# Optimization experiments

Hardware: AMD Instinct MI355X
Metric: run time of the kernel (lower is better)

## Reference

```python
import jax, jax.numpy as jnp
import numpy as np

SLIDING_WINDOW = 512  # matches init kwarg
BLOCK_STRIDE = 32     # tokens per cache page


def setup_inputs() -> dict:
    key = jax.random.key(0)
    k0, k1, k2, k3 = jax.random.split(key, 4)
    B, S, HQ, HKV, D = 2, 2048, 32, 8, 128
    nb = S // BLOCK_STRIDE
    q = jax.random.normal(k0, (B, S, HQ, D), jnp.float32)
    k = jax.random.normal(k1, (B, S, HKV, D), jnp.float32)
    v = jax.random.normal(k2, (B, S, HKV, D), jnp.float32)
    sink = jax.random.normal(k3, (HQ,), jnp.float32)
    cache_state = jnp.zeros((B * nb, 2, HKV, BLOCK_STRIDE, D), jnp.float32)
    seq_block_ids = jnp.arange(B * nb, dtype=jnp.int32).reshape(B, nb)
    return {"q": q, "k": k, "v": v, "cache_state": cache_state,
            "seq_block_ids": seq_block_ids, "sink": sink}


def reference(q, k, v, cache_state, seq_block_ids, sink):
    B, S, HQ, D = q.shape
    HKV = k.shape[2]
    G = HQ // HKV  # GQA group size
    stride = cache_state.shape[3]
    nb = S // stride

    # --- write prefill K/V into the paged cache ---
    # pages laid out [num_pages, k/v, HKV, stride, D]
    k_pg = k.reshape(B, nb, stride, HKV, D).transpose(0, 1, 3, 2, 4).reshape(B * nb, HKV, stride, D)
    v_pg = v.reshape(B, nb, stride, HKV, D).transpose(0, 1, 3, 2, 4).reshape(B * nb, HKV, stride, D)
    ids = seq_block_ids.reshape(-1)
    new_cache = cache_state.at[ids, 0].set(k_pg).at[ids, 1].set(v_pg)

    # --- sliding-window causal attention with sink logits (GQA, no repeat) ---
    scale = 1.0 / np.sqrt(D).astype(np.float32)
    qg = q.reshape(B, S, HKV, G, D)
    # scores: [B, HKV, G, Sq, Sk]
    scores = jnp.einsum('bqhgd,bshd->bhgqs', qg, k) * scale
    i = jnp.arange(S)[:, None]
    j = jnp.arange(S)[None, :]
    allowed = (j <= i) & ((i - j) < SLIDING_WINDOW)  # causal banded mask
    neg = jnp.finfo(scores.dtype).min
    scores = jnp.where(allowed, scores, neg)
    # per-head sink logit appended as extra key column, dropped after softmax
    sink_col = jnp.broadcast_to(sink.reshape(HKV, G)[None, :, :, None, None], (B, HKV, G, S, 1))
    probs = jax.nn.softmax(jnp.concatenate([scores, sink_col], axis=-1), axis=-1)[..., :S]
    out = jnp.einsum('bhgqs,bshd->bqhgd', probs, v).reshape(B, S, HQ, D)
    return out, new_cache
```

## Files before the change

kernel.cpp:

```cpp
#include <hip/hip_runtime.h>
#include <hip/hip_bf16.h>
#include <stdint.h>

#define BB 2
#define SS 2048
#define HQ 32
#define HKV 8
#define DD 128
#define WIN 512

typedef __bf16 bf16x8 __attribute__((ext_vector_type(8)));
typedef float f32x16 __attribute__((ext_vector_type(16)));

__device__ __forceinline__ bf16x8 cvt8(float4 a, float4 b, float s) {
  bf16x8 r;
  r[0] = (__bf16)(a.x * s); r[1] = (__bf16)(a.y * s);
  r[2] = (__bf16)(a.z * s); r[3] = (__bf16)(a.w * s);
  r[4] = (__bf16)(b.x * s); r[5] = (__bf16)(b.y * s);
  r[6] = (__bf16)(b.z * s); r[7] = (__bf16)(b.w * s);
  return r;
}

__device__ __forceinline__ uint32_t pk2(float lo, float hi) {
  uint32_t w;
  asm("v_cvt_pk_bf16_f32 %0, %1, %2" : "=v"(w) : "v"(lo), "v"(hi));
  return w;
}

__device__ __forceinline__ unsigned short bfu(float x) {
  union { __bf16 b; unsigned short u; } c; c.b = (__bf16)x; return c.u;
}

#define SWZ(r) ((((r) ^ ((r) >> 3)) & 7) << 4)

__global__ __launch_bounds__(512, 2) void attn_kernel(
    const float* __restrict__ qg, const float* __restrict__ sinkg,
    float* __restrict__ outg,
    const unsigned short* __restrict__ kbg, const unsigned short* __restrict__ vtg)
{
  const int col = (blockIdx.x & 7) + 8 * ((blockIdx.x >> 3) & 1);
  const int rank = blockIdx.x >> 4;
  const int qtile = rank < 24 ? rank + 8 : 31 - rank;
  const int hkv = col & 7, b = col >> 3;
  const int qb = qtile * 64;
  const int tid = threadIdx.x;
  const int wave = tid >> 6, lane = tid & 63;
  const int c5 = lane & 31, hi = lane >> 5;
  const int hq = (hkv << 2) + (wave >> 1);
  const int qw = qb + (wave & 1) * 32;
  const int qrow = qw + c5;

  __shared__ __align__(16) __bf16 Kl[2][64 * 128];
  __shared__ __align__(16) __bf16 Vt[2][128 * 64];

  const float LOG2E = 1.4426950408889634f;
  const float scale = 0.08838834764831845f * LOG2E;
  const float THR = 12.0f;

  bf16x8 qf[8];
  {
    const float* qp = qg + (((size_t)b * SS + qrow) * HQ + hq) * DD + hi * 8;
    #pragma unroll
    for (int ch = 0; ch < 8; ++ch) {
      float4 a = *(const float4*)(qp + ch * 16);
      float4 a2 = *(const float4*)(qp + ch * 16 + 4);
      qf[ch] = cvt8(a, a2, scale);
    }
  }
  const float sk = sinkg[hq] * LOG2E;

  float mm = -1e30f, ll = 0.f;
  f32x16 acc[4];
  #pragma unroll
  for (int d = 0; d < 4; ++d)
    #pragma unroll
    for (int r = 0; r < 16; ++r) acc[d][r] = 0.f;

  const int t0 = (qb > (WIN - 1) ? (qb - (WIN - 1)) : 0) >> 6;
  const int t1 = (qb + 63) >> 6;

  const char* kcol = (const char*)kbg + (size_t)(b * HKV + hkv) * (SS * DD * 2);
  const char* vcol = (const char*)vtg + (size_t)(b * HKV + hkv) * (SS * DD * 2);
  const int p0 = tid * 32;
  const int kr = p0 >> 8, kx = p0 & 255;
  const int vrw = p0 >> 7, vx = p0 & 127;
  const int kd0 = kr * 256 + (kx ^ SWZ(kr)), kd1 = kr * 256 + ((kx + 16) ^ SWZ(kr));
  const int vd0 = vrw * 128 + (vx ^ SWZ(vrw)), vd1 = vrw * 128 + ((vx + 16) ^ SWZ(vrw));

  uint4 ksA, ksB, vsA, vsB;
  auto issue = [&](int t) {
    const char* kt = kcol + (size_t)t * 16384;
    const char* vt = vcol + (size_t)t * 16384;
    ksA = *(const uint4*)(kt + p0); ksB = *(const uint4*)(kt + p0 + 16);
    vsA = *(const uint4*)(vt + p0); vsB = *(const uint4*)(vt + p0 + 16);
  };
  auto commit = [&](int buf) {
    char* kb_ = (char*)&Kl[buf][0]; char* vb_ = (char*)&Vt[buf][0];
    *(uint4*)(kb_ + kd0) = ksA; *(uint4*)(kb_ + kd1) = ksB;
    *(uint4*)(vb_ + vd0) = vsA; *(uint4*)(vb_ + vd1) = vsB;
  };

  issue(t0);
  commit(0);
  __syncthreads();
  int cur = 0;

  const int swA = SWZ(c5);
  const int swB = swA ^ 0x40;

  for (int t = t0; t <= t1; ++t) {
    if (t < t1) issue(t + 1);
    const int kb = t << 6;

    if (kb <= qw + 31 && kb + 63 >= qw - (WIN - 1)) {
      const char* Ksc = (const char*)&Kl[cur][0];
      const char* Vsc = (const char*)&Vt[cur][0];

      f32x16 s0, s1;
      #pragma unroll
      for (int r = 0; r < 16; ++r) { s0[r] = 0.f; s1[r] = 0.f; }
      __builtin_amdgcn_s_setprio(1);
      #pragma unroll
      for (int ch = 0; ch < 8; ++ch) {
        const int colb = ch * 32 + hi * 16;
        bf16x8 a0 = *(const bf16x8*)(Ksc + c5 * 256 + (colb ^ swA));
        bf16x8 a1 = *(const bf16x8*)(Ksc + (32 + c5) * 256 + (colb ^ swB));
        s0 = __builtin_amdgcn_mfma_f32_32x32x16_bf16(a0, qf[ch], s0, 0, 0, 0);
        s1 = __builtin_amdgcn_mfma_f32_32x32x16_bf16(a1, qf[ch], s1, 0, 0, 0);
      }
      __builtin_amdgcn_s_setprio(0);

      const bool noMask = (kb + 63 <= qw) && (kb >= qw - (WIN - 32));

      if (!noMask) {
        #pragma unroll
        for (int r = 0; r < 16; ++r) {
          const int lr = (r & 3) + 8 * (r >> 2) + 4 * hi;
          const int kv0 = kb + lr, kv1 = kv0 + 32;
          const bool ok0 = (kv0 <= qrow) && (qrow - kv0 < WIN);
          const bool ok1 = (kv1 <= qrow) && (qrow - kv1 < WIN);
          s0[r] = ok0 ? s0[r] : -1e30f;
          s1[r] = ok1 ? s1[r] : -1e30f;
        }
      }
      float tmax = s0[0];
      #pragma unroll
      for (int r = 1; r < 16; ++r) tmax = fmaxf(tmax, s0[r]);
      #pragma unroll
      for (int r = 0; r < 16; ++r) tmax = fmaxf(tmax, s1[r]);
      tmax = fmaxf(tmax, __shfl_xor(tmax, 32));

      const bool resc = __any(tmax > mm + THR);
      const float mnew = resc ? fmaxf(mm, tmax) : mm;
      float tsum = 0.f;
      if (noMask) {
        #pragma unroll
        for (int r = 0; r < 16; ++r) {
          s0[r] = exp2f(s0[r] - mnew); tsum += s0[r];
          s1[r] = exp2f(s1[r] - mnew); tsum += s1[r];
        }
      } else {
        #pragma unroll
        for (int r = 0; r < 16; ++r) {
          s0[r] = (s0[r] > -9e29f) ? exp2f(s0[r] - mnew) : 0.f; tsum += s0[r];
          s1[r] = (s1[r] > -9e29f) ? exp2f(s1[r] - mnew) : 0.f; tsum += s1[r];
        }
      }
      tsum += __shfl_xor(tsum, 32);

      if (resc) {
        const float scl = exp2f(mm - mnew);
        ll = ll * scl + tsum;
        #pragma unroll
        for (int d = 0; d < 4; ++d)
          #pragma unroll
          for (int r = 0; r < 16; ++r) acc[d][r] *= scl;
        mm = mnew;
      } else {
        ll += tsum;
      }

      bf16x8 pb[4];
      #pragma unroll
      for (int kvq = 0; kvq < 4; ++kvq) {
        const int bq = (kvq & 1) * 8;
        float e0, e1, e2, e3, e4, e5, e6, e7;
        if (kvq & 2) {
          e0 = s1[bq+0]; e1 = s1[bq+1]; e2 = s1[bq+2]; e3 = s1[bq+3];
          e4 = s1[bq+4]; e5 = s1[bq+5]; e6 = s1[bq+6]; e7 = s1[bq+7];
        } else {
          e0 = s0[bq+0]; e1 = s0[bq+1]; e2 = s0[bq+2]; e3 = s0[bq+3];
          e4 = s0[bq+4]; e5 = s0[bq+5]; e6 = s0[bq+6]; e7 = s0[bq+7];
        }
        const uint32_t A0 = pk2(e0, e1), A1 = pk2(e2, e3);
        const uint32_t B0 = pk2(e4, e5), B1 = pk2(e6, e7);
        const uint32_t XA0 = __shfl_xor(A0, 32), XA1 = __shfl_xor(A1, 32);
        const uint32_t XB0 = __shfl_xor(B0, 32), XB1 = __shfl_xor(B1, 32);
        union { uint4 u; bf16x8 v; } cvu;
        cvu.u.x = hi ? XB0 : A0;
        cvu.u.y = hi ? XB1 : A1;
        cvu.u.z = hi ? B0 : XA0;
        cvu.u.w = hi ? B1 : XA1;
        pb[kvq] = cvu.v;
      }

      __builtin_amdgcn_s_setprio(1);
      #pragma unroll
      for (int d = 0; d < 4; ++d) {
        const int rowb = (d * 32 + c5) * 128;
        const int swV = swA ^ ((d & 1) << 6);
        #pragma unroll
        for (int kvq = 0; kvq < 4; ++kvq) {
          bf16x8 va = *(const bf16x8*)(Vsc + rowb + ((kvq * 32 + hi * 16) ^ swV));
          acc[d] = __builtin_amdgcn_mfma_f32_32x32x16_bf16(va, pb[kvq], acc[d], 0, 0, 0);
        }
      }
      __builtin_amdgcn_s_setprio(0);
    }

    if (t < t1) {
      commit(cur ^ 1);
      __syncthreads();
      cur ^= 1;
    }
  }

  {
    const float Mf = fmaxf(mm, sk);
    const float ex = exp2f(mm - Mf);
    const float denom = ll * ex + exp2f(sk - Mf);
    const float fac = ex / denom;
    float* orow = outg + (((size_t)b * SS + qrow) * HQ + hq) * DD;
    #pragma unroll
    for (int d = 0; d < 4; ++d) {
      #pragma unroll
      for (int q4 = 0; q4 < 4; ++q4) {
        float4 o;
        o.x = acc[d][q4 * 4 + 0] * fac;
        o.y = acc[d][q4 * 4 + 1] * fac;
        o.z = acc[d][q4 * 4 + 2] * fac;
        o.w = acc[d][q4 * 4 + 3] * fac;
        *(float4*)(orow + d * 32 + q4 * 8 + 4 * hi) = o;
      }
    }
  }
}

__global__ void prep_kv(const float* __restrict__ kg, const float* __restrict__ vg,
                        unsigned short* __restrict__ kb, unsigned short* __restrict__ vt) {
  const int bx = blockIdx.x;
  const int t = bx & 31, colx = bx >> 5;
  const int b = colx >> 3, hkv = colx & 7;
  const int kbrow = t * 64;
  if (blockIdx.y == 0) {
    #pragma unroll
    for (int i = 0; i < 8; ++i) {
      const int idx = i * 1024 + threadIdx.x * 4;
      const int r = idx >> 7, d = idx & 127;
      float4 v = *(const float4*)(kg + (((size_t)b * SS + kbrow + r) * HKV + hkv) * DD + d);
      ushort4 o = make_ushort4(bfu(v.x), bfu(v.y), bfu(v.z), bfu(v.w));
      *(ushort4*)(kb + ((size_t)colx * SS + kbrow + r) * DD + d) = o;
    }
  } else {
    __shared__ unsigned short Vl[64][132];
    #pragma unroll
    for (int i = 0; i < 8; ++i) {
      const int idx = i * 1024 + threadIdx.x * 4;
      const int kv = idx >> 7, d = idx & 127;
      float4 v = *(const float4*)(vg + (((size_t)b * SS + kbrow + kv) * HKV + hkv) * DD + d);
      Vl[kv][d + 0] = bfu(v.x); Vl[kv][d + 1] = bfu(v.y);
      Vl[kv][d + 2] = bfu(v.z); Vl[kv][d + 3] = bfu(v.w);
    }
    __syncthreads();
    #pragma unroll
    for (int i = 0; i < 8; ++i) {
      const int idx = i * 1024 + threadIdx.x * 4;
      const int d = idx >> 6, kv = idx & 63;
      ushort4 o = make_ushort4(Vl[kv + 0][d], Vl[kv + 1][d], Vl[kv + 2][d], Vl[kv + 3][d]);
      *(ushort4*)(vt + ((size_t)colx * 32 + t) * 8192 + d * 64 + kv) = o;
    }
  }
}

__global__ __launch_bounds__(512, 2) void attn_fallback(
    const float* __restrict__ qg, const float* __restrict__ kg,
    const float* __restrict__ vg, const float* __restrict__ sinkg,
    float* __restrict__ outg)
{
  const int col = (blockIdx.x & 7) + 8 * ((blockIdx.x >> 3) & 1);
  const int rank = blockIdx.x >> 4;
  const int qtile = rank < 24 ? rank + 8 : 31 - rank;
  const int hkv = col & 7, b = col >> 3;
  const int qb = qtile * 64;
  const int tid = threadIdx.x;
  const int wave = tid >> 6, lane = tid & 63;
  const int c5 = lane & 31, hi = lane >> 5;
  const int hq = (hkv << 2) + (wave >> 1);
  const int qw = qb + (wave & 1) * 32;
  const int qrow = qw + c5;

  __shared__ __align__(16) __bf16 Kl[2][64 * 128];
  __shared__ __align__(16) __bf16 Vt[2][128 * 64];

  const float LOG2E = 1.4426950408889634f;
  const float scale = 0.08838834764831845f * LOG2E;
  const float THR = 12.0f;

  bf16x8 qf[8];
  {
    const float* qp = qg + (((size_t)b * SS + qrow) * HQ + hq) * DD + hi * 8;
    #pragma unroll
    for (int ch = 0; ch < 8; ++ch) {
      float4 a = *(const float4*)(qp + ch * 16);
      float4 a2 = *(const float4*)(qp + ch * 16 + 4);
      qf[ch] = cvt8(a, a2, scale);
    }
  }
  const float sk = sinkg[hq] * LOG2E;

  float mm = -1e30f, ll = 0.f;
  f32x16 acc[4];
  #pragma unroll
  for (int d = 0; d < 4; ++d)
    #pragma unroll
    for (int r = 0; r < 16; ++r) acc[d][r] = 0.f;

  const int t0 = (qb > (WIN - 1) ? (qb - (WIN - 1)) : 0) >> 6;
  const int t1 = (qb + 63) >> 6;

  const int krow = tid >> 3, kchunk = tid & 7;
  const int vd = tid & 127, vslot = tid >> 7;
  const size_t KSTEP = (size_t)64 * HKV * DD;
  const float* kBase = kg + (((size_t)b * SS + krow) * HKV + hkv) * DD + kchunk * 16;
  const float* vBase = vg + (((size_t)b * SS + vslot * 16) * HKV + hkv) * DD + vd;

  float4 k0, k1, k2, k3; float vr[16];
  auto issue = [&](int t) {
    const float* kp = kBase + (size_t)t * KSTEP;
    k0 = *(const float4*)(kp);     k1 = *(const float4*)(kp + 4);
    k2 = *(const float4*)(kp + 8); k3 = *(const float4*)(kp + 12);
    const float* vp = vBase + (size_t)t * KSTEP;
    #pragma unroll
    for (int j = 0; j < 16; ++j) vr[j] = vp[(size_t)j * (HKV * DD)];
  };
  const int ksw = SWZ(krow);
  const int vsw = SWZ(vd);
  auto commit = [&](int buf) {
    char* kd = (char*)(&Kl[buf][0]) + krow * 256;
    *(bf16x8*)(kd + ((kchunk * 32) ^ ksw)) = cvt8(k0, k1, 1.f);
    *(bf16x8*)(kd + ((kchunk * 32 + 16) ^ ksw)) = cvt8(k2, k3, 1.f);
    char* vdst = (char*)(&Vt[buf][0]) + vd * 128;
    bf16x8 w0, w1;
    #pragma unroll
    for (int j = 0; j < 8; ++j) { w0[j] = (__bf16)vr[j]; w1[j] = (__bf16)vr[8 + j]; }
    *(bf16x8*)(vdst + ((vslot * 32) ^ vsw)) = w0;
    *(bf16x8*)(vdst + ((vslot * 32 + 16) ^ vsw)) = w1;
  };

  issue(t0);
  commit(0);
  __syncthreads();
  int cur = 0;

  const int swA = SWZ(c5);
  const int swB = swA ^ 0x40;

  for (int t = t0; t <= t1; ++t) {
    if (t < t1) issue(t + 1);
    const int kb = t << 6;
    if (kb <= qw + 31 && kb + 63 >= qw - (WIN - 1)) {
      const char* Ksc = (const char*)&Kl[cur][0];
      const char* Vsc = (const char*)&Vt[cur][0];
      f32x16 s0, s1;
      #pragma unroll
      for (int r = 0; r < 16; ++r) { s0[r] = 0.f; s1[r] = 0.f; }
      __builtin_amdgcn_s_setprio(1);
      #pragma unroll
      for (int ch = 0; ch < 8; ++ch) {
        const int colb = ch * 32 + hi * 16;
        bf16x8 a0 = *(const bf16x8*)(Ksc + c5 * 256 + (colb ^ swA));
        bf16x8 a1 = *(const bf16x8*)(Ksc + (32 + c5) * 256 + (colb ^ swB));
        s0 = __builtin_amdgcn_mfma_f32_32x32x16_bf16(a0, qf[ch], s0, 0, 0, 0);
        s1 = __builtin_amdgcn_mfma_f32_32x32x16_bf16(a1, qf[ch], s1, 0, 0, 0);
      }
      __builtin_amdgcn_s_setprio(0);

      const bool noMask = (kb + 63 <= qw) && (kb >= qw - (WIN - 32));
      if (!noMask) {
        #pragma unroll
        for (int r = 0; r < 16; ++r) {
          const int lr = (r & 3) + 8 * (r >> 2) + 4 * hi;
          const int kv0 = kb + lr, kv1 = kv0 + 32;
          const bool ok0 = (kv0 <= qrow) && (qrow - kv0 < WIN);
          const bool ok1 = (kv1 <= qrow) && (qrow - kv1 < WIN);
          s0[r] = ok0 ? s0[r] : -1e30f;
          s1[r] = ok1 ? s1[r] : -1e30f;
        }
      }
      float tmax = s0[0];
      #pragma unroll
      for (int r = 1; r < 16; ++r) tmax = fmaxf(tmax, s0[r]);
      #pragma unroll
      for (int r = 0; r < 16; ++r) tmax = fmaxf(tmax, s1[r]);
      tmax = fmaxf(tmax, __shfl_xor(tmax, 32));
      const bool resc = __any(tmax > mm + THR);
      const float mnew = resc ? fmaxf(mm, tmax) : mm;
      float tsum = 0.f;
      if (noMask) {
        #pragma unroll
        for (int r = 0; r < 16; ++r) {
          s0[r] = exp2f(s0[r] - mnew); tsum += s0[r];
          s1[r] = exp2f(s1[r] - mnew); tsum += s1[r];
        }
      } else {
        #pragma unroll
        for (int r = 0; r < 16; ++r) {
          s0[r] = (s0[r] > -9e29f) ? exp2f(s0[r] - mnew) : 0.f; tsum += s0[r];
          s1[r] = (s1[r] > -9e29f) ? exp2f(s1[r] - mnew) : 0.f; tsum += s1[r];
        }
      }
      tsum += __shfl_xor(tsum, 32);
      if (resc) {
        const float scl = exp2f(mm - mnew);
        ll = ll * scl + tsum;
        #pragma unroll
        for (int d = 0; d < 4; ++d)
          #pragma unroll
          for (int r = 0; r < 16; ++r) acc[d][r] *= scl;
        mm = mnew;
      } else {
        ll += tsum;
      }
      bf16x8 pb[4];
      #pragma unroll
      for (int kvq = 0; kvq < 4; ++kvq) {
        const int bq = (kvq & 1) * 8;
        float e0, e1, e2, e3, e4, e5, e6, e7;
        if (kvq & 2) {
          e0 = s1[bq+0]; e1 = s1[bq+1]; e2 = s1[bq+2]; e3 = s1[bq+3];
          e4 = s1[bq+4]; e5 = s1[bq+5]; e6 = s1[bq+6]; e7 = s1[bq+7];
        } else {
          e0 = s0[bq+0]; e1 = s0[bq+1]; e2 = s0[bq+2]; e3 = s0[bq+3];
          e4 = s0[bq+4]; e5 = s0[bq+5]; e6 = s0[bq+6]; e7 = s0[bq+7];
        }
        const uint32_t A0 = pk2(e0, e1), A1 = pk2(e2, e3);
        const uint32_t B0 = pk2(e4, e5), B1 = pk2(e6, e7);
        const uint32_t XA0 = __shfl_xor(A0, 32), XA1 = __shfl_xor(A1, 32);
        const uint32_t XB0 = __shfl_xor(B0, 32), XB1 = __shfl_xor(B1, 32);
        union { uint4 u; bf16x8 v; } cvu;
        cvu.u.x = hi ? XB0 : A0;
        cvu.u.y = hi ? XB1 : A1;
        cvu.u.z = hi ? B0 : XA0;
        cvu.u.w = hi ? B1 : XA1;
        pb[kvq] = cvu.v;
      }
      __builtin_amdgcn_s_setprio(1);
      #pragma unroll
      for (int d = 0; d < 4; ++d) {
        const int rowb = (d * 32 + c5) * 128;
        const int swV = swA ^ ((d & 1) << 6);
        #pragma unroll
        for (int kvq = 0; kvq < 4; ++kvq) {
          bf16x8 va = *(const bf16x8*)(Vsc + rowb + ((kvq * 32 + hi * 16) ^ swV));
          acc[d] = __builtin_amdgcn_mfma_f32_32x32x16_bf16(va, pb[kvq], acc[d], 0, 0, 0);
        }
      }
      __builtin_amdgcn_s_setprio(0);
    }
    if (t < t1) {
      commit(cur ^ 1);
      __syncthreads();
      cur ^= 1;
    }
  }
  {
    const float Mf = fmaxf(mm, sk);
    const float ex = exp2f(mm - Mf);
    const float denom = ll * ex + exp2f(sk - Mf);
    const float fac = ex / denom;
    float* orow = outg + (((size_t)b * SS + qrow) * HQ + hq) * DD;
    #pragma unroll
    for (int d = 0; d < 4; ++d) {
      #pragma unroll
      for (int q4 = 0; q4 < 4; ++q4) {
        float4 o;
        o.x = acc[d][q4 * 4 + 0] * fac;
        o.y = acc[d][q4 * 4 + 1] * fac;
        o.z = acc[d][q4 * 4 + 2] * fac;
        o.w = acc[d][q4 * 4 + 3] * fac;
        *(float4*)(orow + d * 32 + q4 * 8 + 4 * hi) = o;
      }
    }
  }
}

__global__ void build_inv(const int* __restrict__ ids, int* __restrict__ inv,
                          int npages, int nslots) {
  const int i = threadIdx.x;
  if (i < npages) inv[i] = -1;
  __syncthreads();
  if (i < nslots) inv[ids[i]] = i;
}

__global__ void page_fill(const float* __restrict__ kg, const float* __restrict__ vg,
                          const float* __restrict__ cache_in, const int* __restrict__ inv,
                          float* __restrict__ cache) {
  const int page = blockIdx.x, half = blockIdx.y;
  const int slot = inv[page];
  float4* d4 = (float4*)cache;
  const size_t dbase = (((size_t)page * 2 + half) * 8) * 1024;
  if (slot >= 0) {
    const int b = slot >> 6, blk = slot & 63;
    const float4* s4 = (const float4*)(half ? vg : kg);
    for (int f = threadIdx.x; f < 8192; f += blockDim.x) {
      const int d = f & 31, s = (f >> 5) & 31, h = f >> 10;
      d4[dbase + (size_t)h * 1024 + s * 32 + d] =
          s4[(((size_t)b * SS + blk * 32 + s) * 8 + h) * 32 + d];
    }
  } else {
    const float4* s4 = (const float4*)cache_in;
    for (int f = threadIdx.x; f < 8192; f += blockDim.x)
      d4[dbase + f] = s4[dbase + f];
  }
}

__global__ void cache_copy(const float* __restrict__ src, float* __restrict__ dst, int n4) {
  const float4* s = (const float4*)src;
  float4* d = (float4*)dst;
  for (int i = blockIdx.x * blockDim.x + threadIdx.x; i < n4; i += gridDim.x * blockDim.x)
    d[i] = s[i];
}
__global__ void cache_scatter(const float* __restrict__ kg, const float* __restrict__ vg,
                              const int* __restrict__ ids, float* __restrict__ cache) {
  const int slot = blockIdx.x;
  const int half = blockIdx.y;
  const int b = slot >> 6, blk = slot & 63;
  const int page = ids[slot];
  const float4* s4 = (const float4*)(half ? vg : kg);
  float4* d4 = (float4*)cache;
  for (int f = threadIdx.x; f < 8192; f += blockDim.x) {
    const int d = f & 31, s = (f >> 5) & 31, h = f >> 10;
    d4[(((size_t)page * 2 + half) * 8 + h) * 1024 + s * 32 + d] =
        s4[(((size_t)b * SS + blk * 32 + s) * 8 + h) * 32 + d];
  }
}

extern "C" void kernel_launch(void* const* d_in, const int* in_sizes, int n_in,
                              void* d_out, int out_size, void* d_ws, size_t ws_size,
                              hipStream_t stream) {
  const float* q = (const float*)d_in[0];
  const float* k = (const float*)d_in[1];
  const float* v = (const float*)d_in[2];
  const float* cache_in = (const float*)d_in[3];
  const int* ids = (const int*)d_in[4];
  const float* sink = (const float*)d_in[5];
  float* out = (float*)d_out;
  float* cache_out = out + (size_t)BB * SS * HQ * DD;

  const int nslots = in_sizes[4];
  const int npages = in_sizes[3] / (2 * HKV * 32 * DD);

  const size_t kvBytes = (size_t)BB * HKV * SS * DD * 2;
  const size_t need = 4096 + 2 * kvBytes;
  const bool smallMaps = (npages <= 1024) && (nslots <= 1024);

  if (ws_size >= need && smallMaps) {
    int* inv = (int*)d_ws;
    unsigned short* kbp = (unsigned short*)((char*)d_ws + 4096);
    unsigned short* vtp = kbp + kvBytes / 2;
    build_inv<<<1, 1024, 0, stream>>>(ids, inv, npages, nslots);
    page_fill<<<dim3(npages, 2), 256, 0, stream>>>(k, v, cache_in, inv, cache_out);
    prep_kv<<<dim3(BB * HKV * 32, 2), 256, 0, stream>>>(k, v, kbp, vtp);
    attn_kernel<<<512, 512, 0, stream>>>(q, sink, out, kbp, vtp);
  } else if (ws_size >= (size_t)npages * sizeof(int) && smallMaps) {
    int* inv = (int*)d_ws;
    build_inv<<<1, 1024, 0, stream>>>(ids, inv, npages, nslots);
    page_fill<<<dim3(npages, 2), 256, 0, stream>>>(k, v, cache_in, inv, cache_out);
    attn_fallback<<<512, 512, 0, stream>>>(q, k, v, sink, out);
  } else {
    cache_copy<<<4096, 256, 0, stream>>>(cache_in, cache_out, (BB * SS * HKV * DD * 2) / 4);
    cache_scatter<<<dim3(BB * 64, 2), 256, 0, stream>>>(k, v, ids, cache_out);
    attn_fallback<<<512, 512, 0, stream>>>(q, k, v, sink, out);
  }
}
```

Before: 107.8 us.

## Pre-swizzle K/V into MFMA fragment order and read directly from global

```diff
diff --git a/kernel.cpp b/kernel.cpp
--- a/kernel.cpp
+++ b/kernel.cpp
@@ -36,7 +36,7 @@
 __global__ __launch_bounds__(512, 2) void attn_kernel(
     const float* __restrict__ qg, const float* __restrict__ sinkg,
     float* __restrict__ outg,
-    const unsigned short* __restrict__ kbg, const unsigned short* __restrict__ vtg)
+    const unsigned short* __restrict__ kfg, const unsigned short* __restrict__ vfg)
 {
   const int col = (blockIdx.x & 7) + 8 * ((blockIdx.x >> 3) & 1);
   const int rank = blockIdx.x >> 4;
@@ -50,9 +50,6 @@
   const int qw = qb + (wave & 1) * 32;
   const int qrow = qw + c5;
 
-  __shared__ __align__(16) __bf16 Kl[2][64 * 128];
-  __shared__ __align__(16) __bf16 Vt[2][128 * 64];
-
   const float LOG2E = 1.4426950408889634f;
   const float scale = 0.08838834764831845f * LOG2E;
   const float THR = 12.0f;
@@ -76,28 +73,262 @@
     #pragma unroll
     for (int r = 0; r < 16; ++r) acc[d][r] = 0.f;
 
+  const int t0 = (qw > (WIN - 1) ? (qw - (WIN - 1)) : 0) >> 6;
+  const int t1 = (qw + 31) >> 6;
+
+  const unsigned short* kcol = kfg + (size_t)(b * HKV + hkv) * (SS * DD);
+  const unsigned short* vcol = vfg + (size_t)(b * HKV + hkv) * (SS * DD);
+  const int l8 = lane * 8;
+
+  for (int t = t0; t <= t1; ++t) {
+    const int kb = t << 6;
+    const unsigned short* kt = kcol + t * 8192;
+    const unsigned short* vt = vcol + t * 8192;
+
+    f32x16 s0, s1;
+    #pragma unroll
+    for (int r = 0; r < 16; ++r) { s0[r] = 0.f; s1[r] = 0.f; }
+    __builtin_amdgcn_s_setprio(1);
+    #pragma unroll
+    for (int ch = 0; ch < 8; ++ch) {
+      bf16x8 a0 = *(const bf16x8*)(kt + ch * 1024 + l8);
+      bf16x8 a1 = *(const bf16x8*)(kt + ch * 1024 + 512 + l8);
+      s0 = __builtin_amdgcn_mfma_f32_32x32x16_bf16(a0, qf[ch], s0, 0, 0, 0);
+      s1 = __builtin_amdgcn_mfma_f32_32x32x16_bf16(a1, qf[ch], s1, 0, 0, 0);
+    }
+    __builtin_amdgcn_s_setprio(0);
+
+    const bool noMask = (kb + 63 <= qw) && (kb >= qw - (WIN - 32));
+
+    if (!noMask) {
+      #pragma unroll
+      for (int r = 0; r < 16; ++r) {
+        const int lr = (r & 3) + 8 * (r >> 2) + 4 * hi;
+        const int kv0 = kb + lr, kv1 = kv0 + 32;
+        const bool ok0 = (kv0 <= qrow) && (qrow - kv0 < WIN);
+        const bool ok1 = (kv1 <= qrow) && (qrow - kv1 < WIN);
+        s0[r] = ok0 ? s0[r] : -1e30f;
+        s1[r] = ok1 ? s1[r] : -1e30f;
+      }
+    }
+    float tmax = s0[0];
+    #pragma unroll
+    for (int r = 1; r < 16; ++r) tmax = fmaxf(tmax, s0[r]);
+    #pragma unroll
+    for (int r = 0; r < 16; ++r) tmax = fmaxf(tmax, s1[r]);
+    tmax = fmaxf(tmax, __shfl_xor(tmax, 32));
+
+    const bool resc = __any(tmax > mm + THR);
+    const float mnew = resc ? fmaxf(mm, tmax) : mm;
+    float tsum = 0.f;
+    if (noMask) {
+      #pragma unroll
+      for (int r = 0; r < 16; ++r) {
+        s0[r] = exp2f(s0[r] - mnew); tsum += s0[r];
+        s1[r] = exp2f(s1[r] - mnew); tsum += s1[r];
+      }
+    } else {
+      #pragma unroll
+      for (int r = 0; r < 16; ++r) {
+        s0[r] = (s0[r] > -9e29f) ? exp2f(s0[r] - mnew) : 0.f; tsum += s0[r];
+        s1[r] = (s1[r] > -9e29f) ? exp2f(s1[r] - mnew) : 0.f; tsum += s1[r];
+      }
+    }
+    tsum += __shfl_xor(tsum, 32);
+
+    if (resc) {
+      const float scl = exp2f(mm - mnew);
+      ll = ll * scl + tsum;
+      #pragma unroll
+      for (int d = 0; d < 4; ++d)
+        #pragma unroll
+        for (int r = 0; r < 16; ++r) acc[d][r] *= scl;
+      mm = mnew;
+    } else {
+      ll += tsum;
+    }
+
+    bf16x8 pb[4];
+    #pragma unroll
+    for (int kvq = 0; kvq < 4; ++kvq) {
+      const int bq = (kvq & 1) * 8;
+      float e0, e1, e2, e3, e4, e5, e6, e7;
+      if (kvq & 2) {
+        e0 = s1[bq+0]; e1 = s1[bq+1]; e2 = s1[bq+2]; e3 = s1[bq+3];
+        e4 = s1[bq+4]; e5 = s1[bq+5]; e6 = s1[bq+6]; e7 = s1[bq+7];
+      } else {
+        e0 = s0[bq+0]; e1 = s0[bq+1]; e2 = s0[bq+2]; e3 = s0[bq+3];
+        e4 = s0[bq+4]; e5 = s0[bq+5]; e6 = s0[bq+6]; e7 = s0[bq+7];
+      }
+      const uint32_t A0 = pk2(e0, e1), A1 = pk2(e2, e3);
+      const uint32_t B0 = pk2(e4, e5), B1 = pk2(e6, e7);
+      const uint32_t XA0 = __shfl_xor(A0, 32), XA1 = __shfl_xor(A1, 32);
+      const uint32_t XB0 = __shfl_xor(B0, 32), XB1 = __shfl_xor(B1, 32);
+      union { uint4 u; bf16x8 v; } cvu;
+      cvu.u.x = hi ? XB0 : A0;
+      cvu.u.y = hi ? XB1 : A1;
+      cvu.u.z = hi ? B0 : XA0;
+      cvu.u.w = hi ? B1 : XA1;
+      pb[kvq] = cvu.v;
+    }
+
+    __builtin_amdgcn_s_setprio(1);
+    #pragma unroll
+    for (int d = 0; d < 4; ++d) {
+      #pragma unroll
+      for (int kvq = 0; kvq < 4; ++kvq) {
+        bf16x8 va = *(const bf16x8*)(vt + (d * 4 + kvq) * 512 + l8);
+        acc[d] = __builtin_amdgcn_mfma_f32_32x32x16_bf16(va, pb[kvq], acc[d], 0, 0, 0);
+      }
+    }
+    __builtin_amdgcn_s_setprio(0);
+  }
+
+  {
+    const float Mf = fmaxf(mm, sk);
+    const float ex = exp2f(mm - Mf);
+    const float denom = ll * ex + exp2f(sk - Mf);
+    const float fac = ex / denom;
+    float* orow = outg + (((size_t)b * SS + qrow) * HQ + hq) * DD;
+    #pragma unroll
+    for (int d = 0; d < 4; ++d) {
+      #pragma unroll
+      for (int q4 = 0; q4 < 4; ++q4) {
+        float4 o;
+        o.x = acc[d][q4 * 4 + 0] * fac;
+        o.y = acc[d][q4 * 4 + 1] * fac;
+        o.z = acc[d][q4 * 4 + 2] * fac;
+        o.w = acc[d][q4 * 4 + 3] * fac;
+        *(float4*)(orow + d * 32 + q4 * 8 + 4 * hi) = o;
+      }
+    }
+  }
+}
+
+__global__ void prep_kv(const float* __restrict__ kg, const float* __restrict__ vg,
+                        unsigned short* __restrict__ kf, unsigned short* __restrict__ vf) {
+  const int bx = blockIdx.x;
+  const int t = bx & 31, colx = bx >> 5;
+  const int b = colx >> 3, hkv = colx & 7;
+  const int kbrow = t * 64;
+  if (blockIdx.y == 0) {
+    unsigned short* dst = kf + (size_t)colx * (SS * DD) + t * 8192;
+    #pragma unroll
+    for (int i = 0; i < 4; ++i) {
+      const int c = i * 256 + threadIdx.x;
+      const int ch = c >> 7, rem = c & 127;
+      const int half = rem >> 6, l = rem & 63;
+      const int c5 = l & 31, h2 = l >> 5;
+      const int row = kbrow + half * 32 + c5;
+      const int d = ch * 16 + h2 * 8;
+      const float* kp = kg + (((size_t)b * SS + row) * HKV + hkv) * DD + d;
+      float4 a = *(const float4*)(kp);
+      float4 a2 = *(const float4*)(kp + 4);
+      union { unsigned short u[8]; uint4 q; } o;
+      o.u[0] = bfu(a.x);  o.u[1] = bfu(a.y);  o.u[2] = bfu(a.z);  o.u[3] = bfu(a.w);
+      o.u[4] = bfu(a2.x); o.u[5] = bfu(a2.y); o.u[6] = bfu(a2.z); o.u[7] = bfu(a2.w);
+      *(uint4*)(dst + (size_t)c * 8) = o.q;
+    }
+  } else {
+    __shared__ unsigned short Vl[64][132];
+    #pragma unroll
+    for (int i = 0; i < 8; ++i) {
+      const int idx = i * 1024 + threadIdx.x * 4;
+      const int kv = idx >> 7, d = idx & 127;
+      float4 v = *(const float4*)(vg + (((size_t)b * SS + kbrow + kv) * HKV + hkv) * DD + d);
+      Vl[kv][d + 0] = bfu(v.x); Vl[kv][d + 1] = bfu(v.y);
+      Vl[kv][d + 2] = bfu(v.z); Vl[kv][d + 3] = bfu(v.w);
+    }
+    __syncthreads();
+    unsigned short* dst = vf + (size_t)colx * (SS * DD) + t * 8192;
+    #pragma unroll
+    for (int i = 0; i < 4; ++i) {
+      const int c = i * 256 + threadIdx.x;
+      const int d4 = c >> 8, kvq = (c >> 6) & 3, l = c & 63;
+      const int c5 = l & 31, h2 = l >> 5;
+      const int kvb = kvq * 16 + h2 * 8;
+      const int dc = d4 * 32 + c5;
+      union { unsigned short u[8]; uint4 q; } o;
+      #pragma unroll
+      for (int j = 0; j < 8; ++j) o.u[j] = Vl[kvb + j][dc];
+      *(uint4*)(dst + (size_t)c * 8) = o.q;
+    }
+  }
+}
+
+__global__ __launch_bounds__(512, 2) void attn_fallback(
+    const float* __restrict__ qg, const float* __restrict__ kg,
+    const float* __restrict__ vg, const float* __restrict__ sinkg,
+    float* __restrict__ outg)
+{
+  const int col = (blockIdx.x & 7) + 8 * ((blockIdx.x >> 3) & 1);
+  const int rank = blockIdx.x >> 4;
+  const int qtile = rank < 24 ? rank + 8 : 31 - rank;
+  const int hkv = col & 7, b = col >> 3;
+  const int qb = qtile * 64;
+  const int tid = threadIdx.x;
+  const int wave = tid >> 6, lane = tid & 63;
+  const int c5 = lane & 31, hi = lane >> 5;
+  const int hq = (hkv << 2) + (wave >> 1);
+  const int qw = qb + (wave & 1) * 32;
+  const int qrow = qw + c5;
+
+  __shared__ __align__(16) __bf16 Kl[2][64 * 128];
+  __shared__ __align__(16) __bf16 Vt[2][128 * 64];
+
+  const float LOG2E = 1.4426950408889634f;
+  const float scale = 0.08838834764831845f * LOG2E;
+  const float THR = 12.0f;
+
+  bf16x8 qf[8];
+  {
+    const float* qp = qg + (((size_t)b * SS + qrow) * HQ + hq) * DD + hi * 8;
+    #pragma unroll
+    for (int ch = 0; ch < 8; ++ch) {
+      float4 a = *(const float4*)(qp + ch * 16);
+      float4 a2 = *(const float4*)(qp + ch * 16 + 4);
+      qf[ch] = cvt8(a, a2, scale);
+    }
+  }
+  const float sk = sinkg[hq] * LOG2E;
+
+  float mm = -1e30f, ll = 0.f;
+  f32x16 acc[4];
+  #pragma unroll
+  for (int d = 0; d < 4; ++d)
+    #pragma unroll
+    for (int r = 0; r < 16; ++r) acc[d][r] = 0.f;
+
   const int t0 = (qb > (WIN - 1) ? (qb - (WIN - 1)) : 0) >> 6;
   const int t1 = (qb + 63) >> 6;
 
-  const char* kcol = (const char*)kbg + (size_t)(b * HKV + hkv) * (SS * DD * 2);
-  const char* vcol = (const char*)vtg + (size_t)(b * HKV + hkv) * (SS * DD * 2);
-  const int p0 = tid * 32;
-  const int kr = p0 >> 8, kx = p0 & 255;
-  const int vrw = p0 >> 7, vx = p0 & 127;
-  const int kd0 = kr * 256 + (kx ^ SWZ(kr)), kd1 = kr * 256 + ((kx + 16) ^ SWZ(kr));
-  const int vd0 = vrw * 128 + (vx ^ SWZ(vrw)), vd1 = vrw * 128 + ((vx + 16) ^ SWZ(vrw));
-
-  uint4 ksA, ksB, vsA, vsB;
+  const int krow = tid >> 3, kchunk = tid & 7;
+  const int vd = tid & 127, vslot = tid >> 7;
+  const size_t KSTEP = (size_t)64 * HKV * DD;
+  const float* kBase = kg + (((size_t)b * SS + krow) * HKV + hkv) * DD + kchunk * 16;
+  const float* vBase = vg + (((size_t)b * SS + vslot * 16) * HKV + hkv) * DD + vd;
+
+  float4 k0, k1, k2, k3; float vr[16];
   auto issue = [&](int t) {
-    const char* kt = kcol + (size_t)t * 16384;
-    const char* vt = vcol + (size_t)t * 16384;
-    ksA = *(const uint4*)(kt + p0); ksB = *(const uint4*)(kt + p0 + 16);
-    vsA = *(const uint4*)(vt + p0); vsB = *(const uint4*)(vt + p0 + 16);
+    const float* kp = kBase + (size_t)t * KSTEP;
+    k0 = *(const float4*)(kp);     k1 = *(const float4*)(kp + 4);
+    k2 = *(const float4*)(kp + 8); k3 = *(const float4*)(kp + 12);
+    const float* vp = vBase + (size_t)t * KSTEP;
+    #pragma unroll
+    for (int j = 0; j < 16; ++j) vr[j] = vp[(size_t)j * (HKV * DD)];
   };
+  const int ksw = SWZ(krow);
+  const int vsw = SWZ(vd);
   auto commit = [&](int buf) {
-    char* kb_ = (char*)&Kl[buf][0]; char* vb_ = (char*)&Vt[buf][0];
-    *(uint4*)(kb_ + kd0) = ksA; *(uint4*)(kb_ + kd1) = ksB;
-    *(uint4*)(vb_ + vd0) = vsA; *(uint4*)(vb_ + vd1) = vsB;
+    char* kd = (char*)(&Kl[buf][0]) + krow * 256;
+    *(bf16x8*)(kd + ((kchunk * 32) ^ ksw)) = cvt8(k0, k1, 1.f);
+    *(bf16x8*)(kd + ((kchunk * 32 + 16) ^ ksw)) = cvt8(k2, k3, 1.f);
+    char* vdst = (char*)(&Vt[buf][0]) + vd * 128;
+    bf16x8 w0, w1;
+    #pragma unroll
+    for (int j = 0; j < 8; ++j) { w0[j] = (__bf16)vr[j]; w1[j] = (__bf16)vr[8 + j]; }
+    *(bf16x8*)(vdst + ((vslot * 32) ^ vsw)) = w0;
+    *(bf16x8*)(vdst + ((vslot * 32 + 16) ^ vsw)) = w1;
   };
 
   issue(t0);
@@ -111,15 +342,12 @@
   for (int t = t0; t <= t1; ++t) {
     if (t < t1) issue(t + 1);
     const int kb = t << 6;
-
     if (kb <= qw + 31 && kb + 63 >= qw - (WIN - 1)) {
       const char* Ksc = (const char*)&Kl[cur][0];
       const char* Vsc = (const char*)&Vt[cur][0];
-
       f32x16 s0, s1;
       #pragma unroll
       for (int r = 0; r < 16; ++r) { s0[r] = 0.f; s1[r] = 0.f; }
-      __builtin_amdgcn_s_setprio(1);
       #pragma unroll
       for (int ch = 0; ch < 8; ++ch) {
         const int colb = ch * 32 + hi * 16;
@@ -128,10 +356,7 @@
         s0 = __builtin_amdgcn_mfma_f32_32x32x16_bf16(a0, qf[ch], s0, 0, 0, 0);
         s1 = __builtin_amdgcn_mfma_f32_32x32x16_bf16(a1, qf[ch], s1, 0, 0, 0);
       }
-      __builtin_amdgcn_s_setprio(0);
-
       const bool noMask = (kb + 63 <= qw) && (kb >= qw - (WIN - 32));
-
       if (!noMask) {
         #pragma unroll
         for (int r = 0; r < 16; ++r) {
@@ -149,25 +374,15 @@
       #pragma unroll
       for (int r = 0; r < 16; ++r) tmax = fmaxf(tmax, s1[r]);
       tmax = fmaxf(tmax, __shfl_xor(tmax, 32));
-
       const bool resc = __any(tmax > mm + THR);
       const float mnew = resc ? fmaxf(mm, tmax) : mm;
       float tsum = 0.f;
-      if (noMask) {
-        #pragma unroll
-        for (int r = 0; r < 16; ++r) {
-          s0[r] = exp2f(s0[r] - mnew); tsum += s0[r];
-          s1[r] = exp2f(s1[r] - mnew); tsum += s1[r];
-        }
-      } else {
-        #pragma unroll
-        for (int r = 0; r < 16; ++r) {
-          s0[r] = (s0[r] > -9e29f) ? exp2f(s0[r] - mnew) : 0.f; tsum += s0[r];
-          s1[r] = (s1[r] > -9e29f) ? exp2f(s1[r] - mnew) : 0.f; tsum += s1[r];
-        }
+      #pragma unroll
+      for (int r = 0; r < 16; ++r) {
+        s0[r] = (s0[r] > -9e29f) ? exp2f(s0[r] - mnew) : 0.f; tsum += s0[r];
+        s1[r] = (s1[r] > -9e29f) ? exp2f(s1[r] - mnew) : 0.f; tsum += s1[r];
       }
       tsum += __shfl_xor(tsum, 32);
-
       if (resc) {
         const float scl = exp2f(mm - mnew);
         ll = ll * scl + tsum;
@@ -179,7 +394,6 @@
       } else {
         ll += tsum;
       }
-
       bf16x8 pb[4];
       #pragma unroll
       for (int kvq = 0; kvq < 4; ++kvq) {
@@ -203,8 +417,6 @@
         cvu.u.w = hi ? B1 : XA1;
         pb[kvq] = cvu.v;
       }
-
-      __builtin_amdgcn_s_setprio(1);
       #pragma unroll
       for (int d = 0; d < 4; ++d) {
         const int rowb = (d * 32 + c5) * 128;
@@ -215,257 +427,6 @@
           acc[d] = __builtin_amdgcn_mfma_f32_32x32x16_bf16(va, pb[kvq], acc[d], 0, 0, 0);
         }
       }
-      __builtin_amdgcn_s_setprio(0);
-    }
-
-    if (t < t1) {
-      commit(cur ^ 1);
-      __syncthreads();
-      cur ^= 1;
-    }
-  }
-
-  {
-    const float Mf = fmaxf(mm, sk);
-    const float ex = exp2f(mm - Mf);
-    const float denom = ll * ex + exp2f(sk - Mf);
-    const float fac = ex / denom;
-    float* orow = outg + (((size_t)b * SS + qrow) * HQ + hq) * DD;
-    #pragma unroll
-    for (int d = 0; d < 4; ++d) {
-      #pragma unroll
-      for (int q4 = 0; q4 < 4; ++q4) {
-        float4 o;
-        o.x = acc[d][q4 * 4 + 0] * fac;
-        o.y = acc[d][q4 * 4 + 1] * fac;
-        o.z = acc[d][q4 * 4 + 2] * fac;
-        o.w = acc[d][q4 * 4 + 3] * fac;
-        *(float4*)(orow + d * 32 + q4 * 8 + 4 * hi) = o;
-      }
-    }
-  }
-}
-
-__global__ void prep_kv(const float* __restrict__ kg, const float* __restrict__ vg,
-                        unsigned short* __restrict__ kb, unsigned short* __restrict__ vt) {
-  const int bx = blockIdx.x;
-  const int t = bx & 31, colx = bx >> 5;
-  const int b = colx >> 3, hkv = colx & 7;
-  const int kbrow = t * 64;
-  if (blockIdx.y == 0) {
-    #pragma unroll
-    for (int i = 0; i < 8; ++i) {
-      const int idx = i * 1024 + threadIdx.x * 4;
-      const int r = idx >> 7, d = idx & 127;
-      float4 v = *(const float4*)(kg + (((size_t)b * SS + kbrow + r) * HKV + hkv) * DD + d);
-      ushort4 o = make_ushort4(bfu(v.x), bfu(v.y), bfu(v.z), bfu(v.w));
-      *(ushort4*)(kb + ((size_t)colx * SS + kbrow + r) * DD + d) = o;
-    }
-  } else {
-    __shared__ unsigned short Vl[64][132];
-    #pragma unroll
-    for (int i = 0; i < 8; ++i) {
-      const int idx = i * 1024 + threadIdx.x * 4;
-      const int kv = idx >> 7, d = idx & 127;
-      float4 v = *(const float4*)(vg + (((size_t)b * SS + kbrow + kv) * HKV + hkv) * DD + d);
-      Vl[kv][d + 0] = bfu(v.x); Vl[kv][d + 1] = bfu(v.y);
-      Vl[kv][d + 2] = bfu(v.z); Vl[kv][d + 3] = bfu(v.w);
-    }
-    __syncthreads();
-    #pragma unroll
-    for (int i = 0; i < 8; ++i) {
-      const int idx = i * 1024 + threadIdx.x * 4;
-      const int d = idx >> 6, kv = idx & 63;
-      ushort4 o = make_ushort4(Vl[kv + 0][d], Vl[kv + 1][d], Vl[kv + 2][d], Vl[kv + 3][d]);
-      *(ushort4*)(vt + ((size_t)colx * 32 + t) * 8192 + d * 64 + kv) = o;
-    }
-  }
-}
-
-__global__ __launch_bounds__(512, 2) void attn_fallback(
-    const float* __restrict__ qg, const float* __restrict__ kg,
-    const float* __restrict__ vg, const float* __restrict__ sinkg,
-    float* __restrict__ outg)
-{
-  const int col = (blockIdx.x & 7) + 8 * ((blockIdx.x >> 3) & 1);
-  const int rank = blockIdx.x >> 4;
-  const int qtile = rank < 24 ? rank + 8 : 31 - rank;
-  const int hkv = col & 7, b = col >> 3;
-  const int qb = qtile * 64;
-  const int tid = threadIdx.x;
-  const int wave = tid >> 6, lane = tid & 63;
-  const int c5 = lane & 31, hi = lane >> 5;
-  const int hq = (hkv << 2) + (wave >> 1);
-  const int qw = qb + (wave & 1) * 32;
-  const int qrow = qw + c5;
-
-  __shared__ __align__(16) __bf16 Kl[2][64 * 128];
-  __shared__ __align__(16) __bf16 Vt[2][128 * 64];
-
-  const float LOG2E = 1.4426950408889634f;
-  const float scale = 0.08838834764831845f * LOG2E;
-  const float THR = 12.0f;
-
-  bf16x8 qf[8];
-  {
-    const float* qp = qg + (((size_t)b * SS + qrow) * HQ + hq) * DD + hi * 8;
-    #pragma unroll
-    for (int ch = 0; ch < 8; ++ch) {
-      float4 a = *(const float4*)(qp + ch * 16);
-      float4 a2 = *(const float4*)(qp + ch * 16 + 4);
-      qf[ch] = cvt8(a, a2, scale);
-    }
-  }
-  const float sk = sinkg[hq] * LOG2E;
-
-  float mm = -1e30f, ll = 0.f;
-  f32x16 acc[4];
-  #pragma unroll
-  for (int d = 0; d < 4; ++d)
-    #pragma unroll
-    for (int r = 0; r < 16; ++r) acc[d][r] = 0.f;
-
-  const int t0 = (qb > (WIN - 1) ? (qb - (WIN - 1)) : 0) >> 6;
-  const int t1 = (qb + 63) >> 6;
-
-  const int krow = tid >> 3, kchunk = tid & 7;
-  const int vd = tid & 127, vslot = tid >> 7;
-  const size_t KSTEP = (size_t)64 * HKV * DD;
-  const float* kBase = kg + (((size_t)b * SS + krow) * HKV + hkv) * DD + kchunk * 16;
-  const float* vBase = vg + (((size_t)b * SS + vslot * 16) * HKV + hkv) * DD + vd;
-
-  float4 k0, k1, k2, k3; float vr[16];
-  auto issue = [&](int t) {
-    const float* kp = kBase + (size_t)t * KSTEP;
-    k0 = *(const float4*)(kp);     k1 = *(const float4*)(kp + 4);
-    k2 = *(const float4*)(kp + 8); k3 = *(const float4*)(kp + 12);
-    const float* vp = vBase + (size_t)t * KSTEP;
-    #pragma unroll
-    for (int j = 0; j < 16; ++j) vr[j] = vp[(size_t)j * (HKV * DD)];
-  };
-  const int ksw = SWZ(krow);
-  const int vsw = SWZ(vd);
-  auto commit = [&](int buf) {
-    char* kd = (char*)(&Kl[buf][0]) + krow * 256;
-    *(bf16x8*)(kd + ((kchunk * 32) ^ ksw)) = cvt8(k0, k1, 1.f);
-    *(bf16x8*)(kd + ((kchunk * 32 + 16) ^ ksw)) = cvt8(k2, k3, 1.f);
-    char* vdst = (char*)(&Vt[buf][0]) + vd * 128;
-    bf16x8 w0, w1;
-    #pragma unroll
-    for (int j = 0; j < 8; ++j) { w0[j] = (__bf16)vr[j]; w1[j] = (__bf16)vr[8 + j]; }
-    *(bf16x8*)(vdst + ((vslot * 32) ^ vsw)) = w0;
-    *(bf16x8*)(vdst + ((vslot * 32 + 16) ^ vsw)) = w1;
-  };
-
-  issue(t0);
-  commit(0);
-  __syncthreads();
-  int cur = 0;
-
-  const int swA = SWZ(c5);
-  const int swB = swA ^ 0x40;
-
-  for (int t = t0; t <= t1; ++t) {
-    if (t < t1) issue(t + 1);
-    const int kb = t << 6;
-    if (kb <= qw + 31 && kb + 63 >= qw - (WIN - 1)) {
-      const char* Ksc = (const char*)&Kl[cur][0];
-      const char* Vsc = (const char*)&Vt[cur][0];
-      f32x16 s0, s1;
-      #pragma unroll
-      for (int r = 0; r < 16; ++r) { s0[r] = 0.f; s1[r] = 0.f; }
-      __builtin_amdgcn_s_setprio(1);
-      #pragma unroll
-      for (int ch = 0; ch < 8; ++ch) {
-        const int colb = ch * 32 + hi * 16;
-        bf16x8 a0 = *(const bf16x8*)(Ksc + c5 * 256 + (colb ^ swA));
-        bf16x8 a1 = *(const bf16x8*)(Ksc + (32 + c5) * 256 + (colb ^ swB));
-        s0 = __builtin_amdgcn_mfma_f32_32x32x16_bf16(a0, qf[ch], s0, 0, 0, 0);
-        s1 = __builtin_amdgcn_mfma_f32_32x32x16_bf16(a1, qf[ch], s1, 0, 0, 0);
-      }
-      __builtin_amdgcn_s_setprio(0);
-
-      const bool noMask = (kb + 63 <= qw) && (kb >= qw - (WIN - 32));
-      if (!noMask) {
-        #pragma unroll
-        for (int r = 0; r < 16; ++r) {
-          const int lr = (r & 3) + 8 * (r >> 2) + 4 * hi;
-          const int kv0 = kb + lr, kv1 = kv0 + 32;
-          const bool ok0 = (kv0 <= qrow) && (qrow - kv0 < WIN);
-          const bool ok1 = (kv1 <= qrow) && (qrow - kv1 < WIN);
-          s0[r] = ok0 ? s0[r] : -1e30f;
-          s1[r] = ok1 ? s1[r] : -1e30f;
-        }
-      }
-      float tmax = s0[0];
-      #pragma unroll
-      for (int r = 1; r < 16; ++r) tmax = fmaxf(tmax, s0[r]);
-      #pragma unroll
-      for (int r = 0; r < 16; ++r) tmax = fmaxf(tmax, s1[r]);
-      tmax = fmaxf(tmax, __shfl_xor(tmax, 32));
-      const bool resc = __any(tmax > mm + THR);
-      const float mnew = resc ? fmaxf(mm, tmax) : mm;
-      float tsum = 0.f;
-      if (noMask) {
-        #pragma unroll
-        for (int r = 0; r < 16; ++r) {
-          s0[r] = exp2f(s0[r] - mnew); tsum += s0[r];
-          s1[r] = exp2f(s1[r] - mnew); tsum += s1[r];
-        }
-      } else {
-        #pragma unroll
-        for (int r = 0; r < 16; ++r) {
-          s0[r] = (s0[r] > -9e29f) ? exp2f(s0[r] - mnew) : 0.f; tsum += s0[r];
-          s1[r] = (s1[r] > -9e29f) ? exp2f(s1[r] - mnew) : 0.f; tsum += s1[r];
-        }
-      }
-      tsum += __shfl_xor(tsum, 32);
-      if (resc) {
-        const float scl = exp2f(mm - mnew);
-        ll = ll * scl + tsum;
-        #pragma unroll
-        for (int d = 0; d < 4; ++d)
-          #pragma unroll
-          for (int r = 0; r < 16; ++r) acc[d][r] *= scl;
-        mm = mnew;
-      } else {
-        ll += tsum;
-      }
-      bf16x8 pb[4];
-      #pragma unroll
-      for (int kvq = 0; kvq < 4; ++kvq) {
-        const int bq = (kvq & 1) * 8;
-        float e0, e1, e2, e3, e4, e5, e6, e7;
-        if (kvq & 2) {
-          e0 = s1[bq+0]; e1 = s1[bq+1]; e2 = s1[bq+2]; e3 = s1[bq+3];
-          e4 = s1[bq+4]; e5 = s1[bq+5]; e6 = s1[bq+6]; e7 = s1[bq+7];
-        } else {
-          e0 = s0[bq+0]; e1 = s0[bq+1]; e2 = s0[bq+2]; e3 = s0[bq+3];
-          e4 = s0[bq+4]; e5 = s0[bq+5]; e6 = s0[bq+6]; e7 = s0[bq+7];
-        }
-        const uint32_t A0 = pk2(e0, e1), A1 = pk2(e2, e3);
-        const uint32_t B0 = pk2(e4, e5), B1 = pk2(e6, e7);
-        const uint32_t XA0 = __shfl_xor(A0, 32), XA1 = __shfl_xor(A1, 32);
-        const uint32_t XB0 = __shfl_xor(B0, 32), XB1 = __shfl_xor(B1, 32);
-        union { uint4 u; bf16x8 v; } cvu;
-        cvu.u.x = hi ? XB0 : A0;
-        cvu.u.y = hi ? XB1 : A1;
-        cvu.u.z = hi ? B0 : XA0;
-        cvu.u.w = hi ? B1 : XA1;
-        pb[kvq] = cvu.v;
-      }
-      __builtin_amdgcn_s_setprio(1);
-      #pragma unroll
-      for (int d = 0; d < 4; ++d) {
-        const int rowb = (d * 32 + c5) * 128;
-        const int swV = swA ^ ((d & 1) << 6);
-        #pragma unroll
-        for (int kvq = 0; kvq < 4; ++kvq) {
-          bf16x8 va = *(const bf16x8*)(Vsc + rowb + ((kvq * 32 + hi * 16) ^ swV));
-          acc[d] = __builtin_amdgcn_mfma_f32_32x32x16_bf16(va, pb[kvq], acc[d], 0, 0, 0);
-        }
-      }
-      __builtin_amdgcn_s_setprio(0);
     }
     if (t < t1) {
       commit(cur ^ 1);
@@ -566,12 +527,12 @@
 
   if (ws_size >= need && smallMaps) {
     int* inv = (int*)d_ws;
-    unsigned short* kbp = (unsigned short*)((char*)d_ws + 4096);
-    unsigned short* vtp = kbp + kvBytes / 2;
+    unsigned short* kfp = (unsigned short*)((char*)d_ws + 4096);
+    unsigned short* vfp = kfp + kvBytes / 2;
     build_inv<<<1, 1024, 0, stream>>>(ids, inv, npages, nslots);
     page_fill<<<dim3(npages, 2), 256, 0, stream>>>(k, v, cache_in, inv, cache_out);
-    prep_kv<<<dim3(BB * HKV * 32, 2), 256, 0, stream>>>(k, v, kbp, vtp);
-    attn_kernel<<<512, 512, 0, stream>>>(q, sink, out, kbp, vtp);
+    prep_kv<<<dim3(BB * HKV * 32, 2), 256, 0, stream>>>(k, v, kfp, vfp);
+    attn_kernel<<<512, 512, 0, stream>>>(q, sink, out, kfp, vfp);
   } else if (ws_size >= (size_t)npages * sizeof(int) && smallMaps) {
     int* inv = (int*)d_ws;
     build_inv<<<1, 1024, 0, stream>>>(ids, inv, npages, nslots);
```

Result: slower. 130.9 us (+21.4%).
